# Performance work log

Measured on AMD Instinct MI355X. Metric: run time of the kernel, lower is better.

## Reference

```python
import jax, jax.numpy as jnp
import numpy as np

DIM = 768
HEADS = 12
DH = DIM // HEADS  # 64


def setup_inputs() -> dict:
    key = jax.random.key(0)
    k1, k2, k3, k4, k5 = jax.random.split(key, 5)
    b, p = 16, 1024
    x = jax.random.normal(k1, (b, p, DIM), dtype=jnp.float32)
    # torch nn.Linear params: W [out, in], b [out]
    s_qkv = 1.0 / np.sqrt(DIM)
    Wqkv = jax.random.uniform(k2, (3 * DIM, DIM), jnp.float32, -s_qkv, s_qkv)
    bqkv = jax.random.uniform(k3, (3 * DIM,), jnp.float32, -s_qkv, s_qkv)
    Wo = jax.random.uniform(k4, (DIM, DIM), jnp.float32, -s_qkv, s_qkv)
    bo = jax.random.uniform(k5, (DIM,), jnp.float32, -s_qkv, s_qkv)
    return {"x": x, "Wqkv": Wqkv, "bqkv": bqkv, "Wo": Wo, "bo": bo}


def reference(x, Wqkv, bqkv, Wo, bo):
    b, p, _ = x.shape
    qkv = x @ Wqkv.T + bqkv                      # [b, p, 3*dim]
    q, k, v = jnp.split(qkv, 3, axis=-1)
    def to_heads(t):
        return t.reshape(b, p, HEADS, DH).transpose(0, 2, 1, 3)  # [b, h, p, d]
    q, k, v = to_heads(q), to_heads(k), to_heads(v)
    A = jnp.einsum('bhqd,bhkd->bhqk', q, k) / jnp.sqrt(jnp.float32(DH))
    # NOTE: softmax over the QUERY axis (dim=2), not the key axis
    P = jax.nn.softmax(A, axis=2)                # [b, h, q, k]
    MSA = jnp.einsum('bhqk,bhkd->bhqd', P, v)    # [b, h, p, d]
    MSA = MSA.transpose(0, 2, 1, 3).reshape(b, p, DIM)
    return MSA @ Wo.T + bo
```

## Files before the change

### kernel.cpp

```cpp
#include <hip/hip_runtime.h>
#include <hip/hip_bf16.h>
#include <math.h>

#define DIMC 768
#define HEADS 12
#define DHD 64
#define NB 16
#define NP 1024
#define NQKV (3*DIMC)

typedef __attribute__((ext_vector_type(8))) short bf16x8;
typedef __attribute__((ext_vector_type(4))) float f32x4;

__device__ __forceinline__ short f2bf(float f){
  unsigned u = __builtin_bit_cast(unsigned, f);
  u = (u + 0x7fffu + ((u >> 16) & 1u)) >> 16;
  return (short)u;
}
__device__ __forceinline__ float bf2f(short s){
  return __builtin_bit_cast(float, ((unsigned)(unsigned short)s) << 16);
}
__device__ __forceinline__ bf16x8 cvt8(float4 a, float4 b){
  bf16x8 v;
  v[0]=f2bf(a.x); v[1]=f2bf(a.y); v[2]=f2bf(a.z); v[3]=f2bf(a.w);
  v[4]=f2bf(b.x); v[5]=f2bf(b.y); v[6]=f2bf(b.z); v[7]=f2bf(b.w);
  return v;
}
__device__ __forceinline__ void glds16(const void* gsrc, void* ldst){
  __builtin_amdgcn_global_load_lds(
      (const __attribute__((address_space(1))) unsigned int*)gsrc,
      (__attribute__((address_space(3))) unsigned int*)ldst, 16, 0, 0);
}
__device__ __forceinline__ int xcd_swz(int p, int nwg){
  return (p & 7) * (nwg >> 3) + (p >> 3);
}

__global__ __launch_bounds__(256) void cvt_bf16(const float* __restrict__ in, short* __restrict__ out, int n8)
{
  int i = blockIdx.x*256 + threadIdx.x;
  if (i < n8) {
    float4 f0 = ((const float4*)in)[i*2];
    float4 f1 = ((const float4*)in)[i*2+1];
    ((bf16x8*)out)[i] = cvt8(f0, f1);
  }
}

template<int BCVT, int OUTBF16, int QSCALE>
__global__ __launch_bounds__(256) void gemm_bt(
    const short* __restrict__ A, const void* __restrict__ Bp,
    const float* __restrict__ bias, void* __restrict__ Cp,
    int N, int K, int NX)
{
  __shared__ __align__(16) short As[128*32];
  __shared__ __align__(16) short Bs[128*32];
  const int l = xcd_swz(blockIdx.x, gridDim.x);
  const int bn = (l % NX) * 128, bm = (l / NX) * 128;
  const int t = threadIdx.x;
  const int lane = t & 63, w = t >> 6;
  const int wr = w >> 1, wc = w & 1;
  const int lr = lane & 15, lg = lane >> 4;
  const int srow = lane >> 2;
  const int acol = (lane & 3) * 8;

  f32x4 acc[4][4] = {};

  for (int k0 = 0; k0 < K; k0 += 32) {
    glds16(A + (size_t)(bm + w*32 +  0 + srow)*K + k0 + acol, &As[(w*32 +  0)*32]);
    glds16(A + (size_t)(bm + w*32 + 16 + srow)*K + k0 + acol, &As[(w*32 + 16)*32]);
    if (BCVT) {
      const float* wp = (const float*)Bp + (size_t)(bn + (t>>1))*K + k0 + (t&1)*16;
      float4 f0 = ((const float4*)wp)[0];
      float4 f1 = ((const float4*)wp)[1];
      float4 f2 = ((const float4*)wp)[2];
      float4 f3 = ((const float4*)wp)[3];
      *(bf16x8*)&Bs[(t>>1)*32 + (t&1)*16]     = cvt8(f0, f1);
      *(bf16x8*)&Bs[(t>>1)*32 + (t&1)*16 + 8] = cvt8(f2, f3);
    } else {
      const short* bq = (const short*)Bp;
      glds16(bq + (size_t)(bn + w*32 +  0 + srow)*K + k0 + acol, &Bs[(w*32 +  0)*32]);
      glds16(bq + (size_t)(bn + w*32 + 16 + srow)*K + k0 + acol, &Bs[(w*32 + 16)*32]);
    }
    __syncthreads();
    bf16x8 a[4], b[4];
    #pragma unroll
    for (int i=0;i<4;i++) a[i] = *(const bf16x8*)&As[(wr*64 + i*16 + lr)*32 + lg*8];
    #pragma unroll
    for (int i=0;i<4;i++) b[i] = *(const bf16x8*)&Bs[(wc*64 + i*16 + lr)*32 + lg*8];
    #pragma unroll
    for (int mf=0;mf<4;mf++)
      #pragma unroll
      for (int nf=0;nf<4;nf++)
        acc[mf][nf] = __builtin_amdgcn_mfma_f32_16x16x32_bf16(a[mf], b[nf], acc[mf][nf], 0,0,0);
    __syncthreads();
  }
  #pragma unroll
  for (int nf=0;nf<4;nf++){
    const int n = bn + wc*64 + nf*16 + lr;
    const float bb = bias[n];
    const float sc = (QSCALE && n < DIMC) ? 0.18033688011112042f : 1.0f;
    #pragma unroll
    for (int mf=0;mf<4;mf++)
      #pragma unroll
      for (int i=0;i<4;i++){
        const int m = bm + wr*64 + mf*16 + lg*4 + i;
        const float v = (acc[mf][nf][i] + bb) * sc;
        if (OUTBF16) ((short*)Cp)[(size_t)m*N + n] = f2bf(v);
        else         ((float*)Cp)[(size_t)m*N + n] = v;
      }
  }
}

__global__ __launch_bounds__(256) void vtrans(const short* __restrict__ qkv,
                                              const float* __restrict__ invs,
                                              short* __restrict__ vT)
{
  __shared__ __align__(16) short Ts[64][72];
  __shared__ float invl[64];
  const int pt = blockIdx.x, h = blockIdx.y, b = blockIdx.z;
  const int t = threadIdx.x;
  const size_t bh = (size_t)(b*HEADS + h);
  if (t < 64) invl[t] = invs[bh*NP + pt*64 + t];
  {
    const int r = t >> 2, q = t & 3;
    const short* src = qkv + (size_t)(b*NP + pt*64 + r)*NQKV + 2*DIMC + h*DHD + q*16;
    *(bf16x8*)&Ts[r][q*16]   = *(const bf16x8*)src;
    *(bf16x8*)&Ts[r][q*16+8] = *(const bf16x8*)(src+8);
  }
  __syncthreads();
  {
    const int d = t >> 2, q = t & 3;
    __align__(16) short tmp[16];
    #pragma unroll
    for (int j=0;j<16;j++) tmp[j] = f2bf(bf2f(Ts[q*16 + j][d]) * invl[q*16 + j]);
    short* dst = vT + (bh*DHD + d)*NP + pt*64 + q*16;
    *(bf16x8*)dst     = *(bf16x8*)&tmp[0];
    *(bf16x8*)(dst+8) = *(bf16x8*)&tmp[8];
  }
}

__global__ __launch_bounds__(256) void col_stats(const short* __restrict__ qkv, float* __restrict__ invs)
{
  __shared__ __align__(16) short Ks[128][72];
  __shared__ __align__(16) short Qs[64][72];
  __shared__ float red[4][128];
  const int l = xcd_swz(blockIdx.x, gridDim.x);
  const int kc = l & 7, h = (l >> 3) % HEADS, b = l / (8*HEADS);
  const int t = threadIdx.x;
  const int lane = t & 63, w = t >> 6;
  const int lr = lane & 15, lg = lane >> 4, lk = lg*8;
  const size_t rowbase = (size_t)(b*NP)*NQKV + h*DHD;
  {
    const int r = t >> 1, half = t & 1;
    const short* src = qkv + rowbase + (size_t)(kc*128 + r)*NQKV + DIMC + half*32;
    #pragma unroll
    for (int c=0;c<4;c++)
      *(bf16x8*)&Ks[r][half*32 + c*8] = *(const bf16x8*)(src + c*8);
  }
  float rsum[8] = {};
  for (int qt=0; qt<16; qt++){
    __syncthreads();
    {
      const int r = t >> 2, q = t & 3;
      const short* src = qkv + rowbase + (size_t)(qt*64 + r)*NQKV + q*16;
      *(bf16x8*)&Qs[r][q*16]   = *(const bf16x8*)src;
      *(bf16x8*)&Qs[r][q*16+8] = *(const bf16x8*)(src+8);
    }
    __syncthreads();
    bf16x8 qa0 = *(const bf16x8*)&Qs[w*16 + lr][lk];
    bf16x8 qa1 = *(const bf16x8*)&Qs[w*16 + lr][32 + lk];
    #pragma unroll
    for (int kf=0; kf<8; kf++){
      f32x4 acc = {};
      bf16x8 kb0 = *(const bf16x8*)&Ks[kf*16 + lr][lk];
      bf16x8 kb1 = *(const bf16x8*)&Ks[kf*16 + lr][32 + lk];
      acc = __builtin_amdgcn_mfma_f32_16x16x32_bf16(qa0, kb0, acc, 0,0,0);
      acc = __builtin_amdgcn_mfma_f32_16x16x32_bf16(qa1, kb1, acc, 0,0,0);
      #pragma unroll
      for (int i=0;i<4;i++) rsum[kf] += exp2f(acc[i]);
    }
  }
  #pragma unroll
  for (int kf=0;kf<8;kf++){
    float v = rsum[kf];
    v += __shfl_xor(v, 16);
    v += __shfl_xor(v, 32);
    if (lane < 16) red[w][kf*16 + lr] = v;
  }
  __syncthreads();
  if (t < 128) {
    float s = red[0][t] + red[1][t] + red[2][t] + red[3][t];
    invs[(size_t)(b*HEADS + h)*NP + kc*128 + t] = 1.0f / s;
  }
}

__global__ __launch_bounds__(256) void attn_pv(const short* __restrict__ qkv, const short* __restrict__ vT,
                                               short* __restrict__ msa)
{
  __shared__ __align__(16) short Qs[128][72];
  __shared__ __align__(16) short Ks[64][72];
  __shared__ __align__(16) short Vs[64][72];
  __shared__ __align__(16) short Ps[4][16][72];
  const int l = xcd_swz(blockIdx.x, gridDim.x);
  const int qt2 = l & 7, h = (l >> 3) % HEADS, b = l / (8*HEADS);
  const int t = threadIdx.x;
  const int lane = t & 63, w = t >> 6;
  const int lr = lane & 15, lg = lane >> 4, lk = lg*8;
  const size_t qkvbase = (size_t)(b*NP)*NQKV + h*DHD;
  const size_t bh = (size_t)(b*HEADS + h);
  {
    const int r = t >> 1, half = t & 1;
    const short* src = qkv + qkvbase + (size_t)(qt2*128 + r)*NQKV + half*32;
    *(bf16x8*)&Qs[r][half*32]     = *(const bf16x8*)src;
    *(bf16x8*)&Qs[r][half*32 + 8] = *(const bf16x8*)(src+8);
    *(bf16x8*)&Qs[r][half*32 +16] = *(const bf16x8*)(src+16);
    *(bf16x8*)&Qs[r][half*32 +24] = *(const bf16x8*)(src+24);
  }
  __syncthreads();
  bf16x8 qa[2][2];
  #pragma unroll
  for (int g=0; g<2; g++){
    qa[g][0] = *(const bf16x8*)&Qs[w*32 + g*16 + lr][lk];
    qa[g][1] = *(const bf16x8*)&Qs[w*32 + g*16 + lr][32 + lk];
  }
  f32x4 o[2][4] = {};
  for (int kt=0; kt<16; kt++){
    __syncthreads();
    {
      const int r = t >> 2, q = t & 3;
      const short* ksrc = qkv + qkvbase + (size_t)(kt*64 + r)*NQKV + DIMC + q*16;
      *(bf16x8*)&Ks[r][q*16]   = *(const bf16x8*)ksrc;
      *(bf16x8*)&Ks[r][q*16+8] = *(const bf16x8*)(ksrc+8);
      const short* vsrc = vT + (bh*DHD + r)*NP + kt*64 + q*16;
      *(bf16x8*)&Vs[r][q*16]   = *(const bf16x8*)vsrc;
      *(bf16x8*)&Vs[r][q*16+8] = *(const bf16x8*)(vsrc+8);
    }
    __syncthreads();
    #pragma unroll
    for (int g=0; g<2; g++){
      f32x4 s[4];
      #pragma unroll
      for (int kf=0;kf<4;kf++){
        f32x4 a = {};
        bf16x8 kb0 = *(const bf16x8*)&Ks[kf*16 + lr][lk];
        bf16x8 kb1 = *(const bf16x8*)&Ks[kf*16 + lr][32 + lk];
        a = __builtin_amdgcn_mfma_f32_16x16x32_bf16(qa[g][0], kb0, a, 0,0,0);
        a = __builtin_amdgcn_mfma_f32_16x16x32_bf16(qa[g][1], kb1, a, 0,0,0);
        s[kf] = a;
      }
      #pragma unroll
      for (int kf=0;kf<4;kf++)
        #pragma unroll
        for (int i=0;i<4;i++)
          Ps[w][lg*4 + i][kf*16 + lr] = f2bf(exp2f(s[kf][i]));
      bf16x8 pa0 = *(const bf16x8*)&Ps[w][lr][lk];
      bf16x8 pa1 = *(const bf16x8*)&Ps[w][lr][32 + lk];
      #pragma unroll
      for (int df=0;df<4;df++){
        bf16x8 vb0 = *(const bf16x8*)&Vs[df*16 + lr][lk];
        bf16x8 vb1 = *(const bf16x8*)&Vs[df*16 + lr][32 + lk];
        o[g][df] = __builtin_amdgcn_mfma_f32_16x16x32_bf16(pa0, vb0, o[g][df], 0,0,0);
        o[g][df] = __builtin_amdgcn_mfma_f32_16x16x32_bf16(pa1, vb1, o[g][df], 0,0,0);
      }
    }
  }
  #pragma unroll
  for (int g=0; g<2; g++)
    #pragma unroll
    for (int df=0;df<4;df++){
      const int d = h*DHD + df*16 + lr;
      #pragma unroll
      for (int i=0;i<4;i++){
        const int p = qt2*128 + w*32 + g*16 + lg*4 + i;
        msa[((size_t)(b*NP) + p)*DIMC + d] = f2bf(o[g][df][i]);
      }
    }
}

extern "C" void kernel_launch(void* const* d_in, const int* in_sizes, int n_in,
                              void* d_out, int out_size, void* d_ws, size_t ws_size,
                              hipStream_t stream)
{
  const float* x    = (const float*)d_in[0];
  const float* Wqkv = (const float*)d_in[1];
  const float* bqkv = (const float*)d_in[2];
  const float* Wo   = (const float*)d_in[3];
  const float* bo   = (const float*)d_in[4];
  char* ws = (char*)d_ws;
  short* qkv   = (short*)ws;
  short* vT    = (short*)(ws + 75497472);
  short* Wqkvb = vT;
  short* msa   = (short*)(ws + 100663296);
  short* xb    = msa;
  float* invs  = (float*)(ws + 125829120);

  cvt_bf16<<<6144, 256, 0, stream>>>(x, xb, (16384*768)/8);
  cvt_bf16<<<864, 256, 0, stream>>>(Wqkv, Wqkvb, (2304*768)/8);
  gemm_bt<0,1,1><<<2304, 256, 0, stream>>>(xb, Wqkvb, bqkv, qkv, NQKV, DIMC, 18);
  col_stats<<<1536, 256, 0, stream>>>(qkv, invs);
  vtrans<<<dim3(16, HEADS, NB), 256, 0, stream>>>(qkv, invs, vT);
  attn_pv<<<1536, 256, 0, stream>>>(qkv, vT, msa);
  gemm_bt<1,0,0><<<768, 256, 0, stream>>>(msa, Wo, bo, d_out, DIMC, DIMC, 6);
}
```

Before: 408.2 us.

## Load attention operands straight to registers and pre-convert Wo to bf16

```diff
diff --git a/kernel.cpp b/kernel.cpp
--- a/kernel.cpp
+++ b/kernel.cpp
@@ -45,9 +45,9 @@
   }
 }
 
-template<int BCVT, int OUTBF16, int QSCALE>
+template<int OUTBF16, int QSCALE>
 __global__ __launch_bounds__(256) void gemm_bt(
-    const short* __restrict__ A, const void* __restrict__ Bp,
+    const short* __restrict__ A, const short* __restrict__ B,
     const float* __restrict__ bias, void* __restrict__ Cp,
     int N, int K, int NX)
 {
@@ -67,19 +67,8 @@
   for (int k0 = 0; k0 < K; k0 += 32) {
     glds16(A + (size_t)(bm + w*32 +  0 + srow)*K + k0 + acol, &As[(w*32 +  0)*32]);
     glds16(A + (size_t)(bm + w*32 + 16 + srow)*K + k0 + acol, &As[(w*32 + 16)*32]);
-    if (BCVT) {
-      const float* wp = (const float*)Bp + (size_t)(bn + (t>>1))*K + k0 + (t&1)*16;
-      float4 f0 = ((const float4*)wp)[0];
-      float4 f1 = ((const float4*)wp)[1];
-      float4 f2 = ((const float4*)wp)[2];
-      float4 f3 = ((const float4*)wp)[3];
-      *(bf16x8*)&Bs[(t>>1)*32 + (t&1)*16]     = cvt8(f0, f1);
-      *(bf16x8*)&Bs[(t>>1)*32 + (t&1)*16 + 8] = cvt8(f2, f3);
-    } else {
-      const short* bq = (const short*)Bp;
-      glds16(bq + (size_t)(bn + w*32 +  0 + srow)*K + k0 + acol, &Bs[(w*32 +  0)*32]);
-      glds16(bq + (size_t)(bn + w*32 + 16 + srow)*K + k0 + acol, &Bs[(w*32 + 16)*32]);
-    }
+    glds16(B + (size_t)(bn + w*32 +  0 + srow)*K + k0 + acol, &Bs[(w*32 +  0)*32]);
+    glds16(B + (size_t)(bn + w*32 + 16 + srow)*K + k0 + acol, &Bs[(w*32 + 16)*32]);
     __syncthreads();
     bf16x8 a[4], b[4];
     #pragma unroll
@@ -140,41 +129,30 @@
 
 __global__ __launch_bounds__(256) void col_stats(const short* __restrict__ qkv, float* __restrict__ invs)
 {
-  __shared__ __align__(16) short Ks[128][72];
-  __shared__ __align__(16) short Qs[64][72];
   __shared__ float red[4][128];
   const int l = xcd_swz(blockIdx.x, gridDim.x);
   const int kc = l & 7, h = (l >> 3) % HEADS, b = l / (8*HEADS);
   const int t = threadIdx.x;
   const int lane = t & 63, w = t >> 6;
-  const int lr = lane & 15, lg = lane >> 4, lk = lg*8;
+  const int lr = lane & 15, lg = lane >> 4;
   const size_t rowbase = (size_t)(b*NP)*NQKV + h*DHD;
-  {
-    const int r = t >> 1, half = t & 1;
-    const short* src = qkv + rowbase + (size_t)(kc*128 + r)*NQKV + DIMC + half*32;
-    #pragma unroll
-    for (int c=0;c<4;c++)
-      *(bf16x8*)&Ks[r][half*32 + c*8] = *(const bf16x8*)(src + c*8);
-  }
+  bf16x8 kb[8][2];
+  #pragma unroll
+  for (int kf=0; kf<8; kf++)
+    #pragma unroll
+    for (int hh=0; hh<2; hh++)
+      kb[kf][hh] = *(const bf16x8*)(qkv + rowbase + (size_t)(kc*128 + kf*16 + lr)*NQKV + DIMC + hh*32 + lg*8);
   float rsum[8] = {};
-  for (int qt=0; qt<16; qt++){
-    __syncthreads();
-    {
-      const int r = t >> 2, q = t & 3;
-      const short* src = qkv + rowbase + (size_t)(qt*64 + r)*NQKV + q*16;
-      *(bf16x8*)&Qs[r][q*16]   = *(const bf16x8*)src;
-      *(bf16x8*)&Qs[r][q*16+8] = *(const bf16x8*)(src+8);
-    }
-    __syncthreads();
-    bf16x8 qa0 = *(const bf16x8*)&Qs[w*16 + lr][lk];
-    bf16x8 qa1 = *(const bf16x8*)&Qs[w*16 + lr][32 + lk];
+  for (int jj=0; jj<16; jj++){
+    const int sb = w*16 + jj;
+    const short* qrow = qkv + rowbase + (size_t)(sb*16 + lr)*NQKV + lg*8;
+    bf16x8 qa0 = *(const bf16x8*)qrow;
+    bf16x8 qa1 = *(const bf16x8*)(qrow + 32);
     #pragma unroll
     for (int kf=0; kf<8; kf++){
       f32x4 acc = {};
-      bf16x8 kb0 = *(const bf16x8*)&Ks[kf*16 + lr][lk];
-      bf16x8 kb1 = *(const bf16x8*)&Ks[kf*16 + lr][32 + lk];
-      acc = __builtin_amdgcn_mfma_f32_16x16x32_bf16(qa0, kb0, acc, 0,0,0);
-      acc = __builtin_amdgcn_mfma_f32_16x16x32_bf16(qa1, kb1, acc, 0,0,0);
+      acc = __builtin_amdgcn_mfma_f32_16x16x32_bf16(qa0, kb[kf][0], acc, 0,0,0);
+      acc = __builtin_amdgcn_mfma_f32_16x16x32_bf16(qa1, kb[kf][1], acc, 0,0,0);
       #pragma unroll
       for (int i=0;i<4;i++) rsum[kf] += exp2f(acc[i]);
     }
@@ -196,77 +174,65 @@
 __global__ __launch_bounds__(256) void attn_pv(const short* __restrict__ qkv, const short* __restrict__ vT,
                                                short* __restrict__ msa)
 {
-  __shared__ __align__(16) short Qs[128][72];
-  __shared__ __align__(16) short Ks[64][72];
-  __shared__ __align__(16) short Vs[64][72];
   __shared__ __align__(16) short Ps[4][16][72];
   const int l = xcd_swz(blockIdx.x, gridDim.x);
   const int qt2 = l & 7, h = (l >> 3) % HEADS, b = l / (8*HEADS);
   const int t = threadIdx.x;
   const int lane = t & 63, w = t >> 6;
-  const int lr = lane & 15, lg = lane >> 4, lk = lg*8;
+  const int lr = lane & 15, lg = lane >> 4;
   const size_t qkvbase = (size_t)(b*NP)*NQKV + h*DHD;
   const size_t bh = (size_t)(b*HEADS + h);
+  bf16x8 qa[2][2];
   {
-    const int r = t >> 1, half = t & 1;
-    const short* src = qkv + qkvbase + (size_t)(qt2*128 + r)*NQKV + half*32;
-    *(bf16x8*)&Qs[r][half*32]     = *(const bf16x8*)src;
-    *(bf16x8*)&Qs[r][half*32 + 8] = *(const bf16x8*)(src+8);
-    *(bf16x8*)&Qs[r][half*32 +16] = *(const bf16x8*)(src+16);
-    *(bf16x8*)&Qs[r][half*32 +24] = *(const bf16x8*)(src+24);
-  }
-  __syncthreads();
-  bf16x8 qa[2][2];
-  #pragma unroll
-  for (int g=0; g<2; g++){
-    qa[g][0] = *(const bf16x8*)&Qs[w*32 + g*16 + lr][lk];
-    qa[g][1] = *(const bf16x8*)&Qs[w*32 + g*16 + lr][32 + lk];
-  }
+    const short* Qbase = qkv + qkvbase + (size_t)(qt2*128 + w*32 + lr)*NQKV + lg*8;
+    #pragma unroll
+    for (int g=0; g<2; g++)
+      #pragma unroll
+      for (int hh=0; hh<2; hh++)
+        qa[g][hh] = *(const bf16x8*)(Qbase + (size_t)g*16*NQKV + hh*32);
+  }
+  const short* Kbase = qkv + qkvbase + DIMC + (size_t)lr*NQKV + lg*8;
+  const short* Vbase = vT + (bh*DHD + lr)*NP + lg*8;
   f32x4 o[2][4] = {};
   for (int kt=0; kt<16; kt++){
-    __syncthreads();
-    {
-      const int r = t >> 2, q = t & 3;
-      const short* ksrc = qkv + qkvbase + (size_t)(kt*64 + r)*NQKV + DIMC + q*16;
-      *(bf16x8*)&Ks[r][q*16]   = *(const bf16x8*)ksrc;
-      *(bf16x8*)&Ks[r][q*16+8] = *(const bf16x8*)(ksrc+8);
-      const short* vsrc = vT + (bh*DHD + r)*NP + kt*64 + q*16;
-      *(bf16x8*)&Vs[r][q*16]   = *(const bf16x8*)vsrc;
-      *(bf16x8*)&Vs[r][q*16+8] = *(const bf16x8*)(vsrc+8);
+    bf16x8 kb[4][2], vb[4][2];
+    #pragma unroll
+    for (int kf=0; kf<4; kf++)
+      #pragma unroll
+      for (int hh=0; hh<2; hh++)
+        kb[kf][hh] = *(const bf16x8*)(Kbase + (size_t)(kt*64 + kf*16)*NQKV + hh*32);
+    #pragma unroll
+    for (int df=0; df<4; df++)
+      #pragma unroll
+      for (int kk=0; kk<2; kk++)
+        vb[df][kk] = *(const bf16x8*)(Vbase + (size_t)df*16*NP + kt*64 + kk*32);
+    #pragma unroll
+    for (int g=0; g<2; g++){
+      #pragma unroll
+      for (int kf=0; kf<4; kf++){
+        f32x4 s = {};
+        s = __builtin_amdgcn_mfma_f32_16x16x32_bf16(kb[kf][0], qa[g][0], s, 0,0,0);
+        s = __builtin_amdgcn_mfma_f32_16x16x32_bf16(kb[kf][1], qa[g][1], s, 0,0,0);
+        float e0 = exp2f(s[0]), e1 = exp2f(s[1]), e2 = exp2f(s[2]), e3 = exp2f(s[3]);
+        unsigned u0, u1;
+        asm("v_cvt_pk_bf16_f32 %0, %1, %2" : "=v"(u0) : "v"(e0), "v"(e1));
+        asm("v_cvt_pk_bf16_f32 %0, %1, %2" : "=v"(u1) : "v"(e2), "v"(e3));
+        uint2 uu; uu.x = u0; uu.y = u1;
+        *(uint2*)&Ps[w][lr][kf*16 + lg*4] = uu;
+      }
+      bf16x8 pa0 = *(const bf16x8*)&Ps[w][lr][lg*8];
+      bf16x8 pa1 = *(const bf16x8*)&Ps[w][lr][32 + lg*8];
+      #pragma unroll
+      for (int df=0; df<4; df++){
+        o[g][df] = __builtin_amdgcn_mfma_f32_16x16x32_bf16(pa0, vb[df][0], o[g][df], 0,0,0);
+        o[g][df] = __builtin_amdgcn_mfma_f32_16x16x32_bf16(pa1, vb[df][1], o[g][df], 0,0,0);
+      }
     }
-    __syncthreads();
-    #pragma unroll
-    for (int g=0; g<2; g++){
-      f32x4 s[4];
-      #pragma unroll
-      for (int kf=0;kf<4;kf++){
-        f32x4 a = {};
-        bf16x8 kb0 = *(const bf16x8*)&Ks[kf*16 + lr][lk];
-        bf16x8 kb1 = *(const bf16x8*)&Ks[kf*16 + lr][32 + lk];
-        a = __builtin_amdgcn_mfma_f32_16x16x32_bf16(qa[g][0], kb0, a, 0,0,0);
-        a = __builtin_amdgcn_mfma_f32_16x16x32_bf16(qa[g][1], kb1, a, 0,0,0);
-        s[kf] = a;
-      }
-      #pragma unroll
-      for (int kf=0;kf<4;kf++)
-        #pragma unroll
-        for (int i=0;i<4;i++)
-          Ps[w][lg*4 + i][kf*16 + lr] = f2bf(exp2f(s[kf][i]));
-      bf16x8 pa0 = *(const bf16x8*)&Ps[w][lr][lk];
-      bf16x8 pa1 = *(const bf16x8*)&Ps[w][lr][32 + lk];
-      #pragma unroll
-      for (int df=0;df<4;df++){
-        bf16x8 vb0 = *(const bf16x8*)&Vs[df*16 + lr][lk];
-        bf16x8 vb1 = *(const bf16x8*)&Vs[df*16 + lr][32 + lk];
-        o[g][df] = __builtin_amdgcn_mfma_f32_16x16x32_bf16(pa0, vb0, o[g][df], 0,0,0);
-        o[g][df] = __builtin_amdgcn_mfma_f32_16x16x32_bf16(pa1, vb1, o[g][df], 0,0,0);
-      }
-    }
   }
   #pragma unroll
   for (int g=0; g<2; g++)
     #pragma unroll
-    for (int df=0;df<4;df++){
+    for (int df=0; df<4; df++){
       const int d = h*DHD + df*16 + lr;
       #pragma unroll
       for (int i=0;i<4;i++){
@@ -292,12 +258,14 @@
   short* msa   = (short*)(ws + 100663296);
   short* xb    = msa;
   float* invs  = (float*)(ws + 125829120);
+  short* Wob   = qkv;
 
   cvt_bf16<<<6144, 256, 0, stream>>>(x, xb, (16384*768)/8);
   cvt_bf16<<<864, 256, 0, stream>>>(Wqkv, Wqkvb, (2304*768)/8);
-  gemm_bt<0,1,1><<<2304, 256, 0, stream>>>(xb, Wqkvb, bqkv, qkv, NQKV, DIMC, 18);
+  gemm_bt<1,1><<<2304, 256, 0, stream>>>(xb, Wqkvb, bqkv, qkv, NQKV, DIMC, 18);
   col_stats<<<1536, 256, 0, stream>>>(qkv, invs);
   vtrans<<<dim3(16, HEADS, NB), 256, 0, stream>>>(qkv, invs, vT);
   attn_pv<<<1536, 256, 0, stream>>>(qkv, vT, msa);
-  gemm_bt<1,0,0><<<768, 256, 0, stream>>>(msa, Wo, bo, d_out, DIMC, DIMC, 6);
-}
+  cvt_bf16<<<288, 256, 0, stream>>>(Wo, Wob, (768*768)/8);
+  gemm_bt<0,0><<<768, 256, 0, stream>>>(msa, Wob, bo, d_out, DIMC, DIMC, 6);
+}
```

Result: slower. 519.7 us (+27.3%).
